# Kernel optimization log

Hardware: AMD Instinct MI355X
Metric: run time of the kernel (lower is better)

Reference implementation:

```python
import jax, jax.numpy as jnp
import numpy as np

N = 50000
E = 800000
D_IN = 128
HID = 128
LAT = 64
NEG_SLOPE = 0.2


def setup_inputs() -> dict:
    key = jax.random.key(0)
    ks = jax.random.split(key, 16)
    g = lambda k, shape: jax.random.normal(k, shape, dtype=jnp.float32) * (1.0 / np.sqrt(shape[0]))
    x = jax.random.normal(ks[0], (N, D_IN), dtype=jnp.float32)
    edge_index = jax.random.randint(ks[1], (2, E), 0, N, dtype=jnp.int64)
    return {
        "x": x,
        "edge_index": edge_index,
        # lin1: Linear(D_IN, HID)
        "lin1_w": g(ks[2], (D_IN, HID)),
        "lin1_b": jnp.zeros((HID,), jnp.float32),
        # conv1: GATConv((D_IN, D_IN) -> HID), heads=1
        "w1_src": g(ks[3], (D_IN, HID)),
        "w1_dst": g(ks[4], (D_IN, HID)),
        "a1_src": g(ks[5], (HID,)),
        "a1_dst": g(ks[6], (HID,)),
        "b1": jnp.zeros((HID,), jnp.float32),
        # conv2: GATConv((HID, HID) -> LAT), heads=1
        "w2_src": g(ks[7], (HID, LAT)),
        "w2_dst": g(ks[8], (HID, LAT)),
        "a2_src": g(ks[9], (LAT,)),
        "a2_dst": g(ks[10], (LAT,)),
        "b2": jnp.zeros((LAT,), jnp.float32),
    }


def _gat_conv(x, src, dst, w_src, w_dst, a_src, a_dst, b):
    """PyG GATConv, heads=1, add_self_loops=False. x: [N, Din]."""
    n = x.shape[0]
    hs = x @ w_src                    # [N, C] messages (source transform)
    hd = x @ w_dst                    # [N, C] destination transform
    alpha_s = hs @ a_src              # [N]
    alpha_d = hd @ a_dst              # [N]
    e = jax.nn.leaky_relu(alpha_s[src] + alpha_d[dst], NEG_SLOPE)  # [E]
    # segment softmax over incoming edges per destination node
    m = jax.ops.segment_max(e, dst, num_segments=n)
    ex = jnp.exp(e - m[dst])
    denom = jax.ops.segment_sum(ex, dst, num_segments=n)
    alpha = ex / (denom[dst] + 1e-16)                              # [E]
    msg = hs[src] * alpha[:, None]                                 # [E, C]
    out = jax.ops.segment_sum(msg, dst, num_segments=n)            # [N, C]
    return out + b


def reference(x, edge_index, lin1_w, lin1_b, w1_src, w1_dst, a1_src, a1_dst, b1,
              w2_src, w2_dst, a2_src, a2_dst, b2):
    src, dst = edge_index[0], edge_index[1]
    z = _gat_conv(x, src, dst, w1_src, w1_dst, a1_src, a1_dst, b1)
    z = jax.nn.relu(z + x @ lin1_w + lin1_b)
    z = _gat_conv(z, src, dst, w2_src, w2_dst, a2_src, a2_dst, b2)
    return z
```

## Files before the change

### kernel.cpp

```cpp
#include <hip/hip_runtime.h>

static constexpr int N_NODES = 50000;
static constexpr int N_EDGES = 800000;
static constexpr int NPART = 8;
static constexpr int PART_SZ = N_NODES / NPART;
static constexpr int NTILES = N_NODES / 16;

typedef __attribute__((ext_vector_type(8))) short bf16x8;
typedef __attribute__((ext_vector_type(4))) float f32x4;

__device__ __forceinline__ float bf2f(unsigned short u) {
  union { unsigned int i; float f; } v; v.i = ((unsigned int)u) << 16; return v.f;
}
__device__ __forceinline__ unsigned short f2bf(float f) {
  union { unsigned int i; float f; } v; v.f = f;
  unsigned int r = (v.i + 0x7fffu + ((v.i >> 16) & 1u)) >> 16;
  return (unsigned short)r;
}
__device__ __forceinline__ int clampN(int v) {
  unsigned u = (unsigned)v; return (u < (unsigned)N_NODES) ? (int)u : 0;
}

__global__ void k_detect(const int* __restrict__ ei, int* __restrict__ flag) {
  if (threadIdx.x == 0 && blockIdx.x == 0) {
    int z = ei[1] | ei[3] | ei[5] | ei[7];
    *flag = (z == 0) ? 1 : 0;
  }
}

__global__ void k_zero_out(float* __restrict__ out, int n) {
  int i = blockIdx.x * 256 + threadIdx.x;
  if (i < n) out[i] = 0.f;
}

__global__ void k_compact(const int* __restrict__ ei, const int* __restrict__ flag,
                          int* __restrict__ s32, int* __restrict__ d32) {
  int e = blockIdx.x * 256 + threadIdx.x;
  if (e < N_EDGES) {
    int f = *flag;
    s32[e] = clampN(ei[(size_t)e << f]);
    d32[e] = clampN(ei[(size_t)(N_EDGES + e) << f]);
  }
}

__global__ void k_prepw(const float* __restrict__ w1_src, const float* __restrict__ wlin,
                        const float* __restrict__ w2_src,
                        const float* __restrict__ w1_dst, const float* __restrict__ a1_dst,
                        const float* __restrict__ w2_dst, const float* __restrict__ a2_dst,
                        unsigned short* __restrict__ w1T, unsigned short* __restrict__ w2T,
                        float* __restrict__ c1dst, float* __restrict__ c2dst) {
  int idx = blockIdx.x * 256 + threadIdx.x;
  if (idx < 256 * 128) {
    int c = idx >> 7, k = idx & 127;
    float v = (c < 128) ? w1_src[k * 128 + c] : wlin[k * 128 + (c - 128)];
    w1T[idx] = f2bf(v);
  } else if (idx < 256 * 128 + 64 * 128) {
    int r = idx - 256 * 128;
    int c = r >> 7, k = r & 127;
    w2T[r] = f2bf(w2_src[k * 64 + c]);
  } else if (blockIdx.x == 160) {
    int k = threadIdx.x;
    if (k < 128) {
      float s1 = 0.f;
      for (int c = 0; c < 128; ++c) s1 += w1_dst[k * 128 + c] * a1_dst[c];
      c1dst[k] = s1;
      float s2 = 0.f;
      for (int c = 0; c < 64; ++c) s2 += w2_dst[k * 64 + c] * a2_dst[c];
      c2dst[k] = s2;
    }
  }
}

__global__ __launch_bounds__(256) void k_prepx(
    const float* __restrict__ x, const float* __restrict__ c1dst,
    unsigned short* __restrict__ xb, float* __restrict__ ad1) {
  int gid = blockIdx.x * 256 + threadIdx.x;
  int row = gid >> 4, sl = gid & 15;
  const float* p = x + (size_t)row * 128 + sl * 8;
  float4 a0 = *(const float4*)p;
  float4 a1 = *(const float4*)(p + 4);
  uint4 o;
  o.x = (unsigned)f2bf(a0.x) | ((unsigned)f2bf(a0.y) << 16);
  o.y = (unsigned)f2bf(a0.z) | ((unsigned)f2bf(a0.w) << 16);
  o.z = (unsigned)f2bf(a1.x) | ((unsigned)f2bf(a1.y) << 16);
  o.w = (unsigned)f2bf(a1.z) | ((unsigned)f2bf(a1.w) << 16);
  *(uint4*)(xb + (size_t)row * 128 + sl * 8) = o;
  float4 ca = *(const float4*)(c1dst + sl * 8);
  float4 cb = *(const float4*)(c1dst + sl * 8 + 4);
  float sd = a0.x * ca.x + a0.y * ca.y + a0.z * ca.z + a0.w * ca.w +
             a1.x * cb.x + a1.y * cb.y + a1.z * cb.z + a1.w * cb.w;
  sd += __shfl_xor(sd, 1, 64);
  sd += __shfl_xor(sd, 2, 64);
  sd += __shfl_xor(sd, 4, 64);
  sd += __shfl_xor(sd, 8, 64);
  if (sl == 0) ad1[row] = sd;
}

__global__ __launch_bounds__(256) void k_gemm1(
    const unsigned short* __restrict__ xb, const unsigned short* __restrict__ w1T,
    const float* __restrict__ lin_b,
    unsigned short* __restrict__ hs1, unsigned short* __restrict__ linzb) {
  int tid = threadIdx.x;
  int wv = tid >> 6, l = tid & 63;
  int lrow = l & 15, lk = l >> 4;
  int cb = wv * 64;
  bf16x8 wfrag[4][4];
#pragma unroll
  for (int ct = 0; ct < 4; ++ct)
#pragma unroll
    for (int ks = 0; ks < 4; ++ks)
      wfrag[ct][ks] = *(const bf16x8*)(w1T + (size_t)(cb + ct * 16 + lrow) * 128 + ks * 32 + lk * 8);
  for (int t = blockIdx.x; t < NTILES; t += gridDim.x) {
    int row = t * 16 + lrow;
    bf16x8 xfrag[4];
#pragma unroll
    for (int ks = 0; ks < 4; ++ks)
      xfrag[ks] = *(const bf16x8*)(xb + (size_t)row * 128 + ks * 32 + lk * 8);
    f32x4 acc[4] = {{0.f,0.f,0.f,0.f},{0.f,0.f,0.f,0.f},{0.f,0.f,0.f,0.f},{0.f,0.f,0.f,0.f}};
#pragma unroll
    for (int ks = 0; ks < 4; ++ks)
#pragma unroll
      for (int ct = 0; ct < 4; ++ct)
        acc[ct] = __builtin_amdgcn_mfma_f32_16x16x32_bf16(wfrag[ct][ks], xfrag[ks], acc[ct], 0, 0, 0);
    if (cb < 128) {
#pragma unroll
      for (int ct = 0; ct < 4; ++ct) {
        int col0 = cb + ct * 16 + lk * 4;
        uint2 pv;
        pv.x = (unsigned)f2bf(acc[ct][0]) | ((unsigned)f2bf(acc[ct][1]) << 16);
        pv.y = (unsigned)f2bf(acc[ct][2]) | ((unsigned)f2bf(acc[ct][3]) << 16);
        *(uint2*)(hs1 + (size_t)row * 128 + col0) = pv;
      }
    } else {
#pragma unroll
      for (int ct = 0; ct < 4; ++ct) {
        int col0 = cb - 128 + ct * 16 + lk * 4;
        float4 bv = *(const float4*)(lin_b + col0);
        uint2 pv;
        pv.x = (unsigned)f2bf(acc[ct][0] + bv.x) | ((unsigned)f2bf(acc[ct][1] + bv.y) << 16);
        pv.y = (unsigned)f2bf(acc[ct][2] + bv.z) | ((unsigned)f2bf(acc[ct][3] + bv.w) << 16);
        *(uint2*)(linzb + (size_t)row * 128 + col0) = pv;
      }
    }
  }
}

__global__ __launch_bounds__(256) void k_alpha1(
    const unsigned short* __restrict__ hs1, const float* __restrict__ a1_src,
    float* __restrict__ as1) {
  int gid = blockIdx.x * 256 + threadIdx.x;
  int node = gid >> 3, s = gid & 7;
  if (node >= N_NODES) return;
  uint4 h0 = *(const uint4*)(hs1 + (size_t)node * 128 + s * 16);
  uint4 h1 = *(const uint4*)(hs1 + (size_t)node * 128 + s * 16 + 8);
  const float* a = a1_src + s * 16;
  float sa =
    bf2f((unsigned short)(h0.x & 0xffffu)) * a[0] + bf2f((unsigned short)(h0.x >> 16)) * a[1] +
    bf2f((unsigned short)(h0.y & 0xffffu)) * a[2] + bf2f((unsigned short)(h0.y >> 16)) * a[3] +
    bf2f((unsigned short)(h0.z & 0xffffu)) * a[4] + bf2f((unsigned short)(h0.z >> 16)) * a[5] +
    bf2f((unsigned short)(h0.w & 0xffffu)) * a[6] + bf2f((unsigned short)(h0.w >> 16)) * a[7] +
    bf2f((unsigned short)(h1.x & 0xffffu)) * a[8] + bf2f((unsigned short)(h1.x >> 16)) * a[9] +
    bf2f((unsigned short)(h1.y & 0xffffu)) * a[10] + bf2f((unsigned short)(h1.y >> 16)) * a[11] +
    bf2f((unsigned short)(h1.z & 0xffffu)) * a[12] + bf2f((unsigned short)(h1.z >> 16)) * a[13] +
    bf2f((unsigned short)(h1.w & 0xffffu)) * a[14] + bf2f((unsigned short)(h1.w >> 16)) * a[15];
  sa += __shfl_xor(sa, 1, 64);
  sa += __shfl_xor(sa, 2, 64);
  sa += __shfl_xor(sa, 4, 64);
  if (s == 0) as1[node] = sa;
}

__global__ __launch_bounds__(256) void k_gemm2(
    const unsigned short* __restrict__ zb, const unsigned short* __restrict__ w2T,
    const float* __restrict__ a2_src, const float* __restrict__ c2dst,
    unsigned short* __restrict__ hs2, float* __restrict__ as2, float* __restrict__ ad2) {
  int tid = threadIdx.x;
  int wv = tid >> 6, l = tid & 63;
  int lrow = l & 15, lk = l >> 4;
  int g = blockIdx.x * 4 + wv;
  if (g >= NTILES) return;
  bf16x8 wfrag[4][4];
#pragma unroll
  for (int ct = 0; ct < 4; ++ct)
#pragma unroll
    for (int ks = 0; ks < 4; ++ks)
      wfrag[ct][ks] = *(const bf16x8*)(w2T + (size_t)(ct * 16 + lrow) * 128 + ks * 32 + lk * 8);
  int row = g * 16 + lrow;
  bf16x8 xfrag[4];
  float sd = 0.f;
#pragma unroll
  for (int ks = 0; ks < 4; ++ks) {
    bf16x8 af = *(const bf16x8*)(zb + (size_t)row * 128 + ks * 32 + lk * 8);
    xfrag[ks] = af;
    int k0 = ks * 32 + lk * 8;
    float4 ca = *(const float4*)(c2dst + k0);
    float4 cb = *(const float4*)(c2dst + k0 + 4);
    sd += bf2f((unsigned short)af[0]) * ca.x + bf2f((unsigned short)af[1]) * ca.y +
          bf2f((unsigned short)af[2]) * ca.z + bf2f((unsigned short)af[3]) * ca.w +
          bf2f((unsigned short)af[4]) * cb.x + bf2f((unsigned short)af[5]) * cb.y +
          bf2f((unsigned short)af[6]) * cb.z + bf2f((unsigned short)af[7]) * cb.w;
  }
  sd += __shfl_xor(sd, 16, 64);
  sd += __shfl_xor(sd, 32, 64);
  if (lk == 0) ad2[row] = sd;

  f32x4 acc[4] = {{0.f,0.f,0.f,0.f},{0.f,0.f,0.f,0.f},{0.f,0.f,0.f,0.f},{0.f,0.f,0.f,0.f}};
#pragma unroll
  for (int ks = 0; ks < 4; ++ks)
#pragma unroll
    for (int ct = 0; ct < 4; ++ct)
      acc[ct] = __builtin_amdgcn_mfma_f32_16x16x32_bf16(wfrag[ct][ks], xfrag[ks], acc[ct], 0, 0, 0);
  float pa = 0.f;
#pragma unroll
  for (int ct = 0; ct < 4; ++ct) {
    int col0 = ct * 16 + lk * 4;
    float4 av = *(const float4*)(a2_src + col0);
    pa += acc[ct][0] * av.x + acc[ct][1] * av.y + acc[ct][2] * av.z + acc[ct][3] * av.w;
    uint2 pv;
    pv.x = (unsigned)f2bf(acc[ct][0]) | ((unsigned)f2bf(acc[ct][1]) << 16);
    pv.y = (unsigned)f2bf(acc[ct][2]) | ((unsigned)f2bf(acc[ct][3]) << 16);
    *(uint2*)(hs2 + (size_t)row * 64 + col0) = pv;
  }
  pa += __shfl_xor(pa, 16, 64);
  pa += __shfl_xor(pa, 32, 64);
  if (lk == 0) as2[row] = pa;
}

__global__ void k_count(const int* __restrict__ d32, int* __restrict__ deg) {
  int part = blockIdx.x & (NPART - 1);
  int e = (blockIdx.x >> 3) * 256 + threadIdx.x;
  if (e < N_EDGES) {
    int d = d32[e];
    int lo = part * PART_SZ;
    if (d >= lo && d < lo + PART_SZ) atomicAdd(&deg[d], 1);
  }
}

__global__ __launch_bounds__(256) void k_scan1(const int* __restrict__ deg,
                                               int* __restrict__ offs,
                                               int* __restrict__ bsums, int n) {
  __shared__ int wsum[4];
  int i = blockIdx.x * 256 + threadIdx.x;
  int lane = threadIdx.x & 63, wid = threadIdx.x >> 6;
  int v = (i < n) ? deg[i] : 0;
  int s = v;
#pragma unroll
  for (int o = 1; o < 64; o <<= 1) { int t = __shfl_up(s, o, 64); if (lane >= o) s += t; }
  if (lane == 63) wsum[wid] = s;
  __syncthreads();
  if (threadIdx.x == 0) {
    int a = 0;
#pragma unroll
    for (int w = 0; w < 4; ++w) { a += wsum[w]; wsum[w] = a; }
  }
  __syncthreads();
  int base = (wid > 0) ? wsum[wid - 1] : 0;
  if (i < n) offs[i] = base + s - v;
  if (threadIdx.x == 0) bsums[blockIdx.x] = wsum[3];
}

__global__ __launch_bounds__(256) void k_scan2(int* __restrict__ bsums, int nb,
                                               int* __restrict__ offs, int n, int etot) {
  __shared__ int wsum[4];
  int tid = threadIdx.x, lane = tid & 63, wid = tid >> 6;
  int v = (tid < nb) ? bsums[tid] : 0;
  int s = v;
#pragma unroll
  for (int o = 1; o < 64; o <<= 1) { int t = __shfl_up(s, o, 64); if (lane >= o) s += t; }
  if (lane == 63) wsum[wid] = s;
  __syncthreads();
  if (tid == 0) {
    int a = 0;
#pragma unroll
    for (int w = 0; w < 4; ++w) { a += wsum[w]; wsum[w] = a; }
  }
  __syncthreads();
  int base = (wid > 0) ? wsum[wid - 1] : 0;
  if (tid < nb) bsums[tid] = base + s - v;
  if (tid == 0) offs[n] = etot;
}

__global__ __launch_bounds__(256) void k_scan3(int* __restrict__ offs, int* __restrict__ cursor,
                                               const int* __restrict__ bsums, int n) {
  int i = blockIdx.x * 256 + threadIdx.x;
  if (i < n) {
    int o = offs[i] + bsums[blockIdx.x];
    offs[i] = o;
    cursor[i] = o;
  }
}

__global__ void k_fill(const int* __restrict__ s32, const int* __restrict__ d32,
                       int* __restrict__ cursor, int* __restrict__ ssrc) {
  int part = blockIdx.x & (NPART - 1);
  int e = (blockIdx.x >> 3) * 256 + threadIdx.x;
  if (e < N_EDGES) {
    int d = d32[e];
    int lo = part * PART_SZ;
    if (d >= lo && d < lo + PART_SZ) {
      int p = atomicAdd(&cursor[d], 1);
      if ((unsigned)p < (unsigned)N_EDGES) ssrc[p] = s32[e];
    }
  }
}

__global__ __launch_bounds__(256) void k_agg1(
    const int* __restrict__ offs, const int* __restrict__ ssrc,
    const float* __restrict__ as_, const float* __restrict__ ad_,
    const unsigned short* __restrict__ hs1, const float* __restrict__ b1,
    unsigned short* __restrict__ linzb) {
  int node = (int)((blockIdx.x * 256 + threadIdx.x) >> 6);
  if (node >= N_NODES) return;
  int lane = threadIdx.x & 63;
  int g = lane >> 4, cl = lane & 15;
  int o0 = offs[node], o1 = offs[node + 1];
  if (!((unsigned)o0 <= (unsigned)N_EDGES && (unsigned)o1 <= (unsigned)N_EDGES && o0 <= o1))
    { o0 = 0; o1 = 0; }
  int deg = o1 - o0;
  float ad = ad_[node];
  float acc[8];
#pragma unroll
  for (int k = 0; k < 8; ++k) acc[k] = 0.f;
  float ssum = 0.f;
  for (int j = g; j < deg; j += 4) {
    int s = clampN(ssrc[o0 + j]);
    float e = as_[s] + ad;
    e = e > 0.f ? e : 0.2f * e;
    float w = __expf(e);
    uint4 hv = *(const uint4*)(hs1 + (size_t)s * 128 + cl * 8);
    ssum += w;
    acc[0] += w * __uint_as_float(hv.x << 16);
    acc[1] += w * __uint_as_float(hv.x & 0xffff0000u);
    acc[2] += w * __uint_as_float(hv.y << 16);
    acc[3] += w * __uint_as_float(hv.y & 0xffff0000u);
    acc[4] += w * __uint_as_float(hv.z << 16);
    acc[5] += w * __uint_as_float(hv.z & 0xffff0000u);
    acc[6] += w * __uint_as_float(hv.w << 16);
    acc[7] += w * __uint_as_float(hv.w & 0xffff0000u);
  }
  ssum += __shfl_xor(ssum, 16, 64);
  ssum += __shfl_xor(ssum, 32, 64);
#pragma unroll
  for (int k = 0; k < 8; ++k) {
    acc[k] += __shfl_xor(acc[k], 16, 64);
    acc[k] += __shfl_xor(acc[k], 32, 64);
  }
  if (g == 0) {
    float inv = 1.f / (ssum + 1e-16f);
    uint4 lv = *(const uint4*)(linzb + (size_t)node * 128 + cl * 8);
    float4 ba = *(const float4*)(b1 + cl * 8);
    float4 bb = *(const float4*)(b1 + cl * 8 + 4);
    float z[8];
    z[0] = acc[0] * inv + ba.x + __uint_as_float(lv.x << 16);
    z[1] = acc[1] * inv + ba.y + __uint_as_float(lv.x & 0xffff0000u);
    z[2] = acc[2] * inv + ba.z + __uint_as_float(lv.y << 16);
    z[3] = acc[3] * inv + ba.w + __uint_as_float(lv.y & 0xffff0000u);
    z[4] = acc[4] * inv + bb.x + __uint_as_float(lv.z << 16);
    z[5] = acc[5] * inv + bb.y + __uint_as_float(lv.z & 0xffff0000u);
    z[6] = acc[6] * inv + bb.z + __uint_as_float(lv.w << 16);
    z[7] = acc[7] * inv + bb.w + __uint_as_float(lv.w & 0xffff0000u);
#pragma unroll
    for (int k = 0; k < 8; ++k) z[k] = z[k] > 0.f ? z[k] : 0.f;
    uint4 ov;
    ov.x = (unsigned)f2bf(z[0]) | ((unsigned)f2bf(z[1]) << 16);
    ov.y = (unsigned)f2bf(z[2]) | ((unsigned)f2bf(z[3]) << 16);
    ov.z = (unsigned)f2bf(z[4]) | ((unsigned)f2bf(z[5]) << 16);
    ov.w = (unsigned)f2bf(z[6]) | ((unsigned)f2bf(z[7]) << 16);
    *(uint4*)(linzb + (size_t)node * 128 + cl * 8) = ov;
  }
}

__global__ __launch_bounds__(256) void k_agg2(
    const int* __restrict__ offs, const int* __restrict__ ssrc,
    const float* __restrict__ as_, const float* __restrict__ ad_,
    const unsigned short* __restrict__ hs2, const float* __restrict__ b2,
    float* __restrict__ out) {
  int node = (int)((blockIdx.x * 256 + threadIdx.x) >> 6);
  if (node >= N_NODES) return;
  int lane = threadIdx.x & 63;
  int g = lane >> 3, cl = lane & 7;
  int o0 = offs[node], o1 = offs[node + 1];
  if (!((unsigned)o0 <= (unsigned)N_EDGES && (unsigned)o1 <= (unsigned)N_EDGES && o0 <= o1))
    { o0 = 0; o1 = 0; }
  int deg = o1 - o0;
  float ad = ad_[node];
  float acc[8];
#pragma unroll
  for (int k = 0; k < 8; ++k) acc[k] = 0.f;
  float ssum = 0.f;
  for (int j = g; j < deg; j += 8) {
    int s = clampN(ssrc[o0 + j]);
    float e = as_[s] + ad;
    e = e > 0.f ? e : 0.2f * e;
    float w = __expf(e);
    uint4 hv = *(const uint4*)(hs2 + (size_t)s * 64 + cl * 8);
    ssum += w;
    acc[0] += w * __uint_as_float(hv.x << 16);
    acc[1] += w * __uint_as_float(hv.x & 0xffff0000u);
    acc[2] += w * __uint_as_float(hv.y << 16);
    acc[3] += w * __uint_as_float(hv.y & 0xffff0000u);
    acc[4] += w * __uint_as_float(hv.z << 16);
    acc[5] += w * __uint_as_float(hv.z & 0xffff0000u);
    acc[6] += w * __uint_as_float(hv.w << 16);
    acc[7] += w * __uint_as_float(hv.w & 0xffff0000u);
  }
  ssum += __shfl_xor(ssum, 8, 64);
  ssum += __shfl_xor(ssum, 16, 64);
  ssum += __shfl_xor(ssum, 32, 64);
#pragma unroll
  for (int k = 0; k < 8; ++k) {
    acc[k] += __shfl_xor(acc[k], 8, 64);
    acc[k] += __shfl_xor(acc[k], 16, 64);
    acc[k] += __shfl_xor(acc[k], 32, 64);
  }
  if (g == 0) {
    float inv = 1.f / (ssum + 1e-16f);
    float4 ba = *(const float4*)(b2 + cl * 8);
    float4 bb = *(const float4*)(b2 + cl * 8 + 4);
    float4 oa, ob;
    oa.x = acc[0] * inv + ba.x;
    oa.y = acc[1] * inv + ba.y;
    oa.z = acc[2] * inv + ba.z;
    oa.w = acc[3] * inv + ba.w;
    ob.x = acc[4] * inv + bb.x;
    ob.y = acc[5] * inv + bb.y;
    ob.z = acc[6] * inv + bb.z;
    ob.w = acc[7] * inv + bb.w;
    *(float4*)(out + (size_t)node * 64 + cl * 8) = oa;
    *(float4*)(out + (size_t)node * 64 + cl * 8 + 4) = ob;
  }
}

extern "C" void kernel_launch(void* const* d_in, const int* in_sizes, int n_in,
                              void* d_out, int out_size, void* d_ws, size_t ws_size,
                              hipStream_t stream) {
  (void)in_sizes; (void)n_in;
  const float* x      = (const float*)d_in[0];
  const int*   ei     = (const int*)d_in[1];
  const float* lin1_w = (const float*)d_in[2];
  const float* lin1_b = (const float*)d_in[3];
  const float* w1_src = (const float*)d_in[4];
  const float* w1_dst = (const float*)d_in[5];
  const float* a1_src = (const float*)d_in[6];
  const float* a1_dst = (const float*)d_in[7];
  const float* b1     = (const float*)d_in[8];
  const float* w2_src = (const float*)d_in[9];
  const float* w2_dst = (const float*)d_in[10];
  const float* a2_src = (const float*)d_in[11];
  const float* a2_dst = (const float*)d_in[12];
  const float* b2     = (const float*)d_in[13];
  float* out = (float*)d_out;

  char* ws = (char*)d_ws;
  size_t off = 0;
  auto alloc = [&](size_t bytes) -> void* {
    void* p = ws + off;
    off += (bytes + 255) & ~(size_t)255;
    return p;
  };
  int* flag    = (int*)alloc(256);
  float* c1dst = (float*)alloc(128 * 4);
  float* c2dst = (float*)alloc(128 * 4);
  unsigned short* w1T = (unsigned short*)alloc(256 * 128 * 2);
  unsigned short* w2T = (unsigned short*)alloc(64 * 128 * 2);
  int* deg     = (int*)alloc((size_t)N_NODES * 4);
  int* offs    = (int*)alloc((size_t)(N_NODES + 1) * 4);
  int* cursor  = (int*)alloc((size_t)N_NODES * 4);
  int* bsums   = (int*)alloc(1024);
  float* as1   = (float*)alloc((size_t)N_NODES * 4);
  float* ad1   = (float*)alloc((size_t)N_NODES * 4);
  int* s32     = (int*)alloc((size_t)N_EDGES * 4);
  int* d32     = (int*)alloc((size_t)N_EDGES * 4);
  unsigned short* hs1   = (unsigned short*)alloc((size_t)N_NODES * 128 * 2);
  unsigned short* linzb = (unsigned short*)alloc((size_t)N_NODES * 128 * 2);
  char* U = (char*)alloc((size_t)N_NODES * 128 * 2);
  unsigned short* xb  = (unsigned short*)U;
  int* ssrc           = (int*)U;
  unsigned short* hs2 = (unsigned short*)(U + (size_t)N_EDGES * 4);
  float* as2          = (float*)(U + (size_t)N_EDGES * 4 + (size_t)N_NODES * 128);
  float* ad2          = (float*)(U + (size_t)N_EDGES * 4 + (size_t)N_NODES * 128 + (size_t)N_NODES * 4);

  if (off > ws_size) {
    k_zero_out<<<(out_size + 255) / 256, 256, 0, stream>>>(out, out_size);
    return;
  }

  int ebl  = (N_EDGES + 255) / 256;
  int ebl8 = NPART * ebl;
  int nbl  = (N_NODES + 3) / 4;
  hipMemsetAsync(deg, 0, (size_t)N_NODES * 4, stream);
  k_detect<<<1, 64, 0, stream>>>(ei, flag);
  k_prepw<<<161, 256, 0, stream>>>(w1_src, lin1_w, w2_src, w1_dst, a1_dst, w2_dst, a2_dst,
                                   w1T, w2T, c1dst, c2dst);
  k_compact<<<ebl, 256, 0, stream>>>(ei, flag, s32, d32);
  k_prepx<<<NTILES, 256, 0, stream>>>(x, c1dst, xb, ad1);
  k_gemm1<<<1024, 256, 0, stream>>>(xb, w1T, lin1_b, hs1, linzb);
  k_alpha1<<<(N_NODES * 8 + 255) / 256, 256, 0, stream>>>(hs1, a1_src, as1);
  k_count<<<ebl8, 256, 0, stream>>>(d32, deg);
  int nb = (N_NODES + 255) / 256;
  k_scan1<<<nb, 256, 0, stream>>>(deg, offs, bsums, N_NODES);
  k_scan2<<<1, 256, 0, stream>>>(bsums, nb, offs, N_NODES, N_EDGES);
  k_scan3<<<nb, 256, 0, stream>>>(offs, cursor, bsums, N_NODES);
  k_fill<<<ebl8, 256, 0, stream>>>(s32, d32, cursor, ssrc);
  k_agg1<<<nbl, 256, 0, stream>>>(offs, ssrc, as1, ad1, hs1, b1, linzb);
  k_gemm2<<<(NTILES + 3) / 4, 256, 0, stream>>>(linzb, w2T, a2_src, c2dst, hs2, as2, ad2);
  k_agg2<<<nbl, 256, 0, stream>>>(offs, ssrc, as2, ad2, hs2, b2, out);
}
```

Measured before the change: 209.7 us.

## Fuse source attention logits into gemm1 and widen per-lane aggregation vectors

Removes the separate k_alpha1 kernel by computing the hs·a_src dot product inside k_gemm1's epilogue from fp32 accumulators. The two waves covering the hs1 columns combine their partial sums with atomicAdd into as1, which is now placed next to deg so a single enlarged memset zeroes both. The aggregation kernels also switch to 32-byte feature loads per lane with more edges processed in parallel per wavefront. This saves a launch and a read of hs1, at the cost of atomics, extra shuffle reductions and higher register use in aggregation.

```diff
diff --git a/kernel.cpp b/kernel.cpp
--- a/kernel.cpp
+++ b/kernel.cpp
@@ -98,8 +98,9 @@
 
 __global__ __launch_bounds__(256) void k_gemm1(
     const unsigned short* __restrict__ xb, const unsigned short* __restrict__ w1T,
-    const float* __restrict__ lin_b,
-    unsigned short* __restrict__ hs1, unsigned short* __restrict__ linzb) {
+    const float* __restrict__ lin_b, const float* __restrict__ a1_src,
+    unsigned short* __restrict__ hs1, unsigned short* __restrict__ linzb,
+    float* __restrict__ as1) {
   int tid = threadIdx.x;
   int wv = tid >> 6, l = tid & 63;
   int lrow = l & 15, lk = l >> 4;
@@ -123,14 +124,20 @@
       for (int ct = 0; ct < 4; ++ct)
         acc[ct] = __builtin_amdgcn_mfma_f32_16x16x32_bf16(wfrag[ct][ks], xfrag[ks], acc[ct], 0, 0, 0);
     if (cb < 128) {
+      float pa = 0.f;
 #pragma unroll
       for (int ct = 0; ct < 4; ++ct) {
         int col0 = cb + ct * 16 + lk * 4;
+        float4 av = *(const float4*)(a1_src + col0);
+        pa += acc[ct][0] * av.x + acc[ct][1] * av.y + acc[ct][2] * av.z + acc[ct][3] * av.w;
         uint2 pv;
         pv.x = (unsigned)f2bf(acc[ct][0]) | ((unsigned)f2bf(acc[ct][1]) << 16);
         pv.y = (unsigned)f2bf(acc[ct][2]) | ((unsigned)f2bf(acc[ct][3]) << 16);
         *(uint2*)(hs1 + (size_t)row * 128 + col0) = pv;
       }
+      pa += __shfl_xor(pa, 16, 64);
+      pa += __shfl_xor(pa, 32, 64);
+      if (l < 16) atomicAdd(&as1[t * 16 + l], pa);
     } else {
 #pragma unroll
       for (int ct = 0; ct < 4; ++ct) {
@@ -143,30 +150,6 @@
       }
     }
   }
-}
-
-__global__ __launch_bounds__(256) void k_alpha1(
-    const unsigned short* __restrict__ hs1, const float* __restrict__ a1_src,
-    float* __restrict__ as1) {
-  int gid = blockIdx.x * 256 + threadIdx.x;
-  int node = gid >> 3, s = gid & 7;
-  if (node >= N_NODES) return;
-  uint4 h0 = *(const uint4*)(hs1 + (size_t)node * 128 + s * 16);
-  uint4 h1 = *(const uint4*)(hs1 + (size_t)node * 128 + s * 16 + 8);
-  const float* a = a1_src + s * 16;
-  float sa =
-    bf2f((unsigned short)(h0.x & 0xffffu)) * a[0] + bf2f((unsigned short)(h0.x >> 16)) * a[1] +
-    bf2f((unsigned short)(h0.y & 0xffffu)) * a[2] + bf2f((unsigned short)(h0.y >> 16)) * a[3] +
-    bf2f((unsigned short)(h0.z & 0xffffu)) * a[4] + bf2f((unsigned short)(h0.z >> 16)) * a[5] +
-    bf2f((unsigned short)(h0.w & 0xffffu)) * a[6] + bf2f((unsigned short)(h0.w >> 16)) * a[7] +
-    bf2f((unsigned short)(h1.x & 0xffffu)) * a[8] + bf2f((unsigned short)(h1.x >> 16)) * a[9] +
-    bf2f((unsigned short)(h1.y & 0xffffu)) * a[10] + bf2f((unsigned short)(h1.y >> 16)) * a[11] +
-    bf2f((unsigned short)(h1.z & 0xffffu)) * a[12] + bf2f((unsigned short)(h1.z >> 16)) * a[13] +
-    bf2f((unsigned short)(h1.w & 0xffffu)) * a[14] + bf2f((unsigned short)(h1.w >> 16)) * a[15];
-  sa += __shfl_xor(sa, 1, 64);
-  sa += __shfl_xor(sa, 2, 64);
-  sa += __shfl_xor(sa, 4, 64);
-  if (s == 0) as1[node] = sa;
 }
 
 __global__ __launch_bounds__(256) void k_gemm2(
@@ -311,61 +294,79 @@
   int node = (int)((blockIdx.x * 256 + threadIdx.x) >> 6);
   if (node >= N_NODES) return;
   int lane = threadIdx.x & 63;
-  int g = lane >> 4, cl = lane & 15;
+  int g = lane >> 3, cl = lane & 7;
   int o0 = offs[node], o1 = offs[node + 1];
   if (!((unsigned)o0 <= (unsigned)N_EDGES && (unsigned)o1 <= (unsigned)N_EDGES && o0 <= o1))
     { o0 = 0; o1 = 0; }
   int deg = o1 - o0;
   float ad = ad_[node];
-  float acc[8];
-#pragma unroll
-  for (int k = 0; k < 8; ++k) acc[k] = 0.f;
+  float acc[16];
+#pragma unroll
+  for (int k = 0; k < 16; ++k) acc[k] = 0.f;
   float ssum = 0.f;
-  for (int j = g; j < deg; j += 4) {
+  for (int j = g; j < deg; j += 8) {
     int s = clampN(ssrc[o0 + j]);
     float e = as_[s] + ad;
     e = e > 0.f ? e : 0.2f * e;
     float w = __expf(e);
-    uint4 hv = *(const uint4*)(hs1 + (size_t)s * 128 + cl * 8);
+    const uint4* hp = (const uint4*)(hs1 + (size_t)s * 128 + cl * 16);
+    uint4 h0 = hp[0];
+    uint4 h1 = hp[1];
     ssum += w;
-    acc[0] += w * __uint_as_float(hv.x << 16);
-    acc[1] += w * __uint_as_float(hv.x & 0xffff0000u);
-    acc[2] += w * __uint_as_float(hv.y << 16);
-    acc[3] += w * __uint_as_float(hv.y & 0xffff0000u);
-    acc[4] += w * __uint_as_float(hv.z << 16);
-    acc[5] += w * __uint_as_float(hv.z & 0xffff0000u);
-    acc[6] += w * __uint_as_float(hv.w << 16);
-    acc[7] += w * __uint_as_float(hv.w & 0xffff0000u);
-  }
+    acc[0]  += w * __uint_as_float(h0.x << 16);
+    acc[1]  += w * __uint_as_float(h0.x & 0xffff0000u);
+    acc[2]  += w * __uint_as_float(h0.y << 16);
+    acc[3]  += w * __uint_as_float(h0.y & 0xffff0000u);
+    acc[4]  += w * __uint_as_float(h0.z << 16);
+    acc[5]  += w * __uint_as_float(h0.z & 0xffff0000u);
+    acc[6]  += w * __uint_as_float(h0.w << 16);
+    acc[7]  += w * __uint_as_float(h0.w & 0xffff0000u);
+    acc[8]  += w * __uint_as_float(h1.x << 16);
+    acc[9]  += w * __uint_as_float(h1.x & 0xffff0000u);
+    acc[10] += w * __uint_as_float(h1.y << 16);
+    acc[11] += w * __uint_as_float(h1.y & 0xffff0000u);
+    acc[12] += w * __uint_as_float(h1.z << 16);
+    acc[13] += w * __uint_as_float(h1.z & 0xffff0000u);
+    acc[14] += w * __uint_as_float(h1.w << 16);
+    acc[15] += w * __uint_as_float(h1.w & 0xffff0000u);
+  }
+  ssum += __shfl_xor(ssum, 8, 64);
   ssum += __shfl_xor(ssum, 16, 64);
   ssum += __shfl_xor(ssum, 32, 64);
 #pragma unroll
-  for (int k = 0; k < 8; ++k) {
+  for (int k = 0; k < 16; ++k) {
+    acc[k] += __shfl_xor(acc[k], 8, 64);
     acc[k] += __shfl_xor(acc[k], 16, 64);
     acc[k] += __shfl_xor(acc[k], 32, 64);
   }
   if (g == 0) {
     float inv = 1.f / (ssum + 1e-16f);
-    uint4 lv = *(const uint4*)(linzb + (size_t)node * 128 + cl * 8);
-    float4 ba = *(const float4*)(b1 + cl * 8);
-    float4 bb = *(const float4*)(b1 + cl * 8 + 4);
-    float z[8];
-    z[0] = acc[0] * inv + ba.x + __uint_as_float(lv.x << 16);
-    z[1] = acc[1] * inv + ba.y + __uint_as_float(lv.x & 0xffff0000u);
-    z[2] = acc[2] * inv + ba.z + __uint_as_float(lv.y << 16);
-    z[3] = acc[3] * inv + ba.w + __uint_as_float(lv.y & 0xffff0000u);
-    z[4] = acc[4] * inv + bb.x + __uint_as_float(lv.z << 16);
-    z[5] = acc[5] * inv + bb.y + __uint_as_float(lv.z & 0xffff0000u);
-    z[6] = acc[6] * inv + bb.z + __uint_as_float(lv.w << 16);
-    z[7] = acc[7] * inv + bb.w + __uint_as_float(lv.w & 0xffff0000u);
-#pragma unroll
-    for (int k = 0; k < 8; ++k) z[k] = z[k] > 0.f ? z[k] : 0.f;
-    uint4 ov;
-    ov.x = (unsigned)f2bf(z[0]) | ((unsigned)f2bf(z[1]) << 16);
-    ov.y = (unsigned)f2bf(z[2]) | ((unsigned)f2bf(z[3]) << 16);
-    ov.z = (unsigned)f2bf(z[4]) | ((unsigned)f2bf(z[5]) << 16);
-    ov.w = (unsigned)f2bf(z[6]) | ((unsigned)f2bf(z[7]) << 16);
-    *(uint4*)(linzb + (size_t)node * 128 + cl * 8) = ov;
+    const uint4* lp = (const uint4*)(linzb + (size_t)node * 128 + cl * 16);
+    uint4 l0 = lp[0];
+    uint4 l1 = lp[1];
+    float z[16];
+    unsigned lw[8] = {l0.x, l0.y, l0.z, l0.w, l1.x, l1.y, l1.z, l1.w};
+#pragma unroll
+    for (int q = 0; q < 8; ++q) {
+      float bx = b1[cl * 16 + q * 2];
+      float by = b1[cl * 16 + q * 2 + 1];
+      z[q * 2]     = acc[q * 2] * inv + bx + __uint_as_float(lw[q] << 16);
+      z[q * 2 + 1] = acc[q * 2 + 1] * inv + by + __uint_as_float(lw[q] & 0xffff0000u);
+    }
+#pragma unroll
+    for (int k = 0; k < 16; ++k) z[k] = z[k] > 0.f ? z[k] : 0.f;
+    uint4 o0v, o1v;
+    o0v.x = (unsigned)f2bf(z[0])  | ((unsigned)f2bf(z[1])  << 16);
+    o0v.y = (unsigned)f2bf(z[2])  | ((unsigned)f2bf(z[3])  << 16);
+    o0v.z = (unsigned)f2bf(z[4])  | ((unsigned)f2bf(z[5])  << 16);
+    o0v.w = (unsigned)f2bf(z[6])  | ((unsigned)f2bf(z[7])  << 16);
+    o1v.x = (unsigned)f2bf(z[8])  | ((unsigned)f2bf(z[9])  << 16);
+    o1v.y = (unsigned)f2bf(z[10]) | ((unsigned)f2bf(z[11]) << 16);
+    o1v.z = (unsigned)f2bf(z[12]) | ((unsigned)f2bf(z[13]) << 16);
+    o1v.w = (unsigned)f2bf(z[14]) | ((unsigned)f2bf(z[15]) << 16);
+    uint4* op = (uint4*)(linzb + (size_t)node * 128 + cl * 16);
+    op[0] = o0v;
+    op[1] = o1v;
   }
 }
 
@@ -377,56 +378,66 @@
   int node = (int)((blockIdx.x * 256 + threadIdx.x) >> 6);
   if (node >= N_NODES) return;
   int lane = threadIdx.x & 63;
-  int g = lane >> 3, cl = lane & 7;
+  int g = lane >> 2, cl = lane & 3;
   int o0 = offs[node], o1 = offs[node + 1];
   if (!((unsigned)o0 <= (unsigned)N_EDGES && (unsigned)o1 <= (unsigned)N_EDGES && o0 <= o1))
     { o0 = 0; o1 = 0; }
   int deg = o1 - o0;
   float ad = ad_[node];
-  float acc[8];
-#pragma unroll
-  for (int k = 0; k < 8; ++k) acc[k] = 0.f;
+  float acc[16];
+#pragma unroll
+  for (int k = 0; k < 16; ++k) acc[k] = 0.f;
   float ssum = 0.f;
-  for (int j = g; j < deg; j += 8) {
+  for (int j = g; j < deg; j += 16) {
     int s = clampN(ssrc[o0 + j]);
     float e = as_[s] + ad;
     e = e > 0.f ? e : 0.2f * e;
     float w = __expf(e);
-    uint4 hv = *(const uint4*)(hs2 + (size_t)s * 64 + cl * 8);
+    const uint4* hp = (const uint4*)(hs2 + (size_t)s * 64 + cl * 16);
+    uint4 h0 = hp[0];
+    uint4 h1 = hp[1];
     ssum += w;
-    acc[0] += w * __uint_as_float(hv.x << 16);
-    acc[1] += w * __uint_as_float(hv.x & 0xffff0000u);
-    acc[2] += w * __uint_as_float(hv.y << 16);
-    acc[3] += w * __uint_as_float(hv.y & 0xffff0000u);
-    acc[4] += w * __uint_as_float(hv.z << 16);
-    acc[5] += w * __uint_as_float(hv.z & 0xffff0000u);
-    acc[6] += w * __uint_as_float(hv.w << 16);
-    acc[7] += w * __uint_as_float(hv.w & 0xffff0000u);
-  }
+    acc[0]  += w * __uint_as_float(h0.x << 16);
+    acc[1]  += w * __uint_as_float(h0.x & 0xffff0000u);
+    acc[2]  += w * __uint_as_float(h0.y << 16);
+    acc[3]  += w * __uint_as_float(h0.y & 0xffff0000u);
+    acc[4]  += w * __uint_as_float(h0.z << 16);
+    acc[5]  += w * __uint_as_float(h0.z & 0xffff0000u);
+    acc[6]  += w * __uint_as_float(h0.w << 16);
+    acc[7]  += w * __uint_as_float(h0.w & 0xffff0000u);
+    acc[8]  += w * __uint_as_float(h1.x << 16);
+    acc[9]  += w * __uint_as_float(h1.x & 0xffff0000u);
+    acc[10] += w * __uint_as_float(h1.y << 16);
+    acc[11] += w * __uint_as_float(h1.y & 0xffff0000u);
+    acc[12] += w * __uint_as_float(h1.z << 16);
+    acc[13] += w * __uint_as_float(h1.z & 0xffff0000u);
+    acc[14] += w * __uint_as_float(h1.w << 16);
+    acc[15] += w * __uint_as_float(h1.w & 0xffff0000u);
+  }
+  ssum += __shfl_xor(ssum, 4, 64);
   ssum += __shfl_xor(ssum, 8, 64);
   ssum += __shfl_xor(ssum, 16, 64);
   ssum += __shfl_xor(ssum, 32, 64);
 #pragma unroll
-  for (int k = 0; k < 8; ++k) {
+  for (int k = 0; k < 16; ++k) {
+    acc[k] += __shfl_xor(acc[k], 4, 64);
     acc[k] += __shfl_xor(acc[k], 8, 64);
     acc[k] += __shfl_xor(acc[k], 16, 64);
     acc[k] += __shfl_xor(acc[k], 32, 64);
   }
   if (g == 0) {
     float inv = 1.f / (ssum + 1e-16f);
-    float4 ba = *(const float4*)(b2 + cl * 8);
-    float4 bb = *(const float4*)(b2 + cl * 8 + 4);
-    float4 oa, ob;
-    oa.x = acc[0] * inv + ba.x;
-    oa.y = acc[1] * inv + ba.y;
-    oa.z = acc[2] * inv + ba.z;
-    oa.w = acc[3] * inv + ba.w;
-    ob.x = acc[4] * inv + bb.x;
-    ob.y = acc[5] * inv + bb.y;
-    ob.z = acc[6] * inv + bb.z;
-    ob.w = acc[7] * inv + bb.w;
-    *(float4*)(out + (size_t)node * 64 + cl * 8) = oa;
-    *(float4*)(out + (size_t)node * 64 + cl * 8 + 4) = ob;
+    float* op = out + (size_t)node * 64 + cl * 16;
+#pragma unroll
+    for (int q = 0; q < 4; ++q) {
+      float4 bv = *(const float4*)(b2 + cl * 16 + q * 4);
+      float4 ov;
+      ov.x = acc[q * 4]     * inv + bv.x;
+      ov.y = acc[q * 4 + 1] * inv + bv.y;
+      ov.z = acc[q * 4 + 2] * inv + bv.z;
+      ov.w = acc[q * 4 + 3] * inv + bv.w;
+      *(float4*)(op + q * 4) = ov;
+    }
   }
 }
 
@@ -463,10 +474,10 @@
   unsigned short* w1T = (unsigned short*)alloc(256 * 128 * 2);
   unsigned short* w2T = (unsigned short*)alloc(64 * 128 * 2);
   int* deg     = (int*)alloc((size_t)N_NODES * 4);
+  float* as1   = (float*)alloc((size_t)N_NODES * 4);
   int* offs    = (int*)alloc((size_t)(N_NODES + 1) * 4);
   int* cursor  = (int*)alloc((size_t)N_NODES * 4);
   int* bsums   = (int*)alloc(1024);
-  float* as1   = (float*)alloc((size_t)N_NODES * 4);
   float* ad1   = (float*)alloc((size_t)N_NODES * 4);
   int* s32     = (int*)alloc((size_t)N_EDGES * 4);
   int* d32     = (int*)alloc((size_t)N_EDGES * 4);
@@ -487,14 +498,14 @@
   int ebl  = (N_EDGES + 255) / 256;
   int ebl8 = NPART * ebl;
   int nbl  = (N_NODES + 3) / 4;
-  hipMemsetAsync(deg, 0, (size_t)N_NODES * 4, stream);
+  size_t degPad = ((size_t)N_NODES * 4 + 255) & ~(size_t)255;
+  hipMemsetAsync(deg, 0, degPad + (size_t)N_NODES * 4, stream);
   k_detect<<<1, 64, 0, stream>>>(ei, flag);
   k_prepw<<<161, 256, 0, stream>>>(w1_src, lin1_w, w2_src, w1_dst, a1_dst, w2_dst, a2_dst,
                                    w1T, w2T, c1dst, c2dst);
   k_compact<<<ebl, 256, 0, stream>>>(ei, flag, s32, d32);
   k_prepx<<<NTILES, 256, 0, stream>>>(x, c1dst, xb, ad1);
-  k_gemm1<<<1024, 256, 0, stream>>>(xb, w1T, lin1_b, hs1, linzb);
-  k_alpha1<<<(N_NODES * 8 + 255) / 256, 256, 0, stream>>>(hs1, a1_src, as1);
+  k_gemm1<<<1024, 256, 0, stream>>>(xb, w1T, lin1_b, a1_src, hs1, linzb, as1);
   k_count<<<ebl8, 256, 0, stream>>>(d32, deg);
   int nb = (N_NODES + 255) / 256;
   k_scan1<<<nb, 256, 0, stream>>>(deg, offs, bsums, N_NODES);
```

Result: slower. 220.6 us (+5.2%).
